# Kernel optimization log

Hardware: AMD Instinct MI355X
Metric: run time of the kernel (lower is better)

Reference implementation:

```python
import jax, jax.numpy as jnp
import numpy as np

B = 128
IN = 256
NLVL = 6
KLVL = 3
CH = 4
C = 4 * CH * CH          # 64 channels per node
OU = 8                   # out_filter_siz_u
OV = 8                   # out_filter_siz_v
NK = 2 ** KLVL           # 8 leaf nodes per axis
W_SCALE = 1.0 / 16.0     # ~1/sqrt(2*2*C) so 7 stacked relu-convs stay numerically sane


def setup_inputs() -> dict:
    key = jax.random.key(0)
    ks = jax.random.split(key, 2 * NLVL + 4)
    fx = IN // 2 ** NLVL  # 4: input patch filter size
    inp = {}
    inp["in_data"] = jax.random.normal(ks[0], (B, IN, IN, 1), jnp.float32)
    inp["in_filter"] = jax.random.normal(ks[1], (fx, fx, 1, C), jnp.float32) * W_SCALE
    inp["in_bias"] = jnp.zeros((C,), jnp.float32)
    i = 2
    for lvl in range(1, NLVL + 1):
        n = 2 ** min(lvl, KLVL)  # node grid: grows to 2^klvl then stays
        inp[f"f{lvl}"] = jax.random.normal(ks[i], (n, n, 2, 2, C, C), jnp.float32) * W_SCALE
        inp[f"b{lvl}"] = jnp.zeros((n, n, C), jnp.float32)
        i += 1
    inp["Wd"] = jax.random.normal(ks[i], (NK, NK, 2, C, OU * OV), jnp.float32) * W_SCALE
    return inp


def _node_conv(x, w, b):
    # x: [Nu,Nv,B,H,W,C]; w: [Nu,Nv,2,2,C,C]; 2x2 stride-2 VALID conv per node
    Nu, Nv, Bn, H, W, Cc = x.shape
    xr = x.reshape(Nu, Nv, Bn, H // 2, 2, W // 2, 2, Cc)
    y = jnp.einsum('uvbhxwyc,uvxyco->uvbhwo', xr, w)
    return jax.nn.relu(y + b[:, :, None, None, None, :])


def _forward(in_data, in_filter, in_bias, fs, bs, Wd):
    Bn = in_data.shape[0]
    fx, fy = in_filter.shape[0], in_filter.shape[1]
    # input interp conv: stride == kernel -> non-overlapping patch GEMM
    xr = in_data[..., 0].reshape(Bn, in_data.shape[1] // fx, fx, in_data.shape[2] // fy, fy)
    x = jax.nn.relu(jnp.einsum('bxpyq,pqc->bxyc', xr, in_filter[:, :, 0, :]) + in_bias)
    x = x[None, None]  # [1,1,B,2^nlvl,2^nlvl,C] node grid
    for lvl in range(1, NLVL + 1):
        if lvl <= KLVL:
            # children (itu,itv) read parent (itu//2, itv//2)
            x = jnp.repeat(jnp.repeat(x, 2, axis=0), 2, axis=1)
        x = _node_conv(x, fs[lvl - 1], bs[lvl - 1])
    feats = x[:, :, :, 0, 0, :]  # [NK,NK,B,C]; spatial is 1x1 at level nlvl
    out = jnp.einsum('uvbc,uvrck->uvbrk', feats, Wd)  # r in {real, imag}
    out = out.reshape(NK, NK, Bn, 2, OU, OV)
    out = jnp.transpose(out, (2, 0, 4, 1, 5, 3))  # [B,itu,ou,itv,ov,2]
    return out.reshape(Bn, NK * OU, NK * OV, 2)


def reference(in_data, in_filter, in_bias, f1, b1, f2, b2, f3, b3, f4, b4, f5, b5, f6, b6, Wd):
    fs = (f1, f2, f3, f4, f5, f6)
    bs = (b1, b2, b3, b4, b5, b6)
    return _forward(in_data, in_filter, in_bias, fs, bs, Wd)
```

## Files before the change

### kernel.cpp

```cpp
#include <hip/hip_runtime.h>
#include <hip/hip_bf16.h>
#include <cstdint>
#include <cstddef>


typedef __attribute__((ext_vector_type(8))) short short8;
typedef __attribute__((ext_vector_type(4))) float f32x4;
typedef unsigned short ushort_t;

static __device__ __forceinline__ float b2f(const __hip_bfloat16 x) {
    return __bfloat162float(x);
}
static __device__ __forceinline__ ushort_t f2bf(float x) {
    __hip_bfloat16 h = __float2bfloat16(x);
    ushort_t u;
    __builtin_memcpy(&u, &h, 2);
    return u;
}
static __device__ __forceinline__ void gl_lds16(const void* g, void* l) {
    __builtin_amdgcn_global_load_lds(
        (const __attribute__((address_space(1))) void*)g,
        (__attribute__((address_space(3))) void*)l, 16, 0, 0);
}

__global__ void k_detect(const uint32_t* __restrict__ in, int* __restrict__ flag) {
    const int t = threadIdx.x;
    const float v = __uint_as_float(in[t]);
    const bool plaus = (v == 0.0f) || (fabsf(v) > 1e-8f && fabsf(v) < 1e4f);
    const unsigned long long m = __ballot(plaus);
    if (t == 0) *flag = (__popcll(m) >= 48) ? 0 : 1;
}

__global__ __launch_bounds__(256) void k_prepw(
    const void* f1, const void* f2, const void* f3,
    const void* f4, const void* f5, const void* f6, const void* wdsrc,
    ushort_t* __restrict__ wbuf, ushort_t* __restrict__ wdbuf,
    const int* __restrict__ flag)
{
    const int isbf = *flag;
    const int gid = blockIdx.x * 256 + threadIdx.x;
    if (gid >= 630784) return;
    if (gid >= 565248) {
        const int local = gid - 565248;
        const int lane = local & 63;
        const int slot = (local >> 6) & 15;
        const int site = local >> 10;
        const int ks2 = slot >> 3, nh = slot & 7, q = lane >> 4;
        const int n = nh * 16 + (lane & 15);
        const int r = n >> 6, kk = n & 63;
        const int cbase = ks2 * 32 + q * 8;
        ushort_t pk[8];
        if (isbf) {
            const ushort_t* s = (const ushort_t*)wdsrc;
            #pragma unroll
            for (int j = 0; j < 8; j++)
                pk[j] = s[(((size_t)(site * 2 + r) * 64 + cbase + j) * 64) + kk];
        } else {
            const float* s = (const float*)wdsrc;
            #pragma unroll
            for (int j = 0; j < 8; j++)
                pk[j] = f2bf(s[(((size_t)(site * 2 + r) * 64 + cbase + j) * 64) + kk]);
        }
        *(uint4*)&wdbuf[(size_t)local * 8] = *(uint4*)pk;
        return;
    }
    const void* fsrc; int base;
    if      (gid <   8192) { fsrc = f1; base = 0;      }
    else if (gid <  40960) { fsrc = f2; base = 8192;   }
    else if (gid < 172032) { fsrc = f3; base = 40960;  }
    else if (gid < 303104) { fsrc = f4; base = 172032; }
    else if (gid < 434176) { fsrc = f5; base = 303104; }
    else                   { fsrc = f6; base = 434176; }
    const int local = gid - base;
    const int lane = local & 63;
    const int slot = (local >> 6) & 7;
    const int sitetap = local >> 9;
    const int ks = slot >> 2, nh = slot & 3, q = lane >> 4;
    const int n = (lane & 15) + nh * 16;
    const int kbase = ks * 32 + q * 8;
    ushort_t pk[8];
    if (isbf) {
        const ushort_t* s = (const ushort_t*)fsrc + (size_t)sitetap * 4096;
        #pragma unroll
        for (int j = 0; j < 8; j++) pk[j] = s[(kbase + j) * 64 + n];
    } else {
        const float* s = (const float*)fsrc + (size_t)sitetap * 4096;
        #pragma unroll
        for (int j = 0; j < 8; j++) pk[j] = f2bf(s[(kbase + j) * 64 + n]);
    }
    *(uint4*)&wbuf[(size_t)gid * 8] = *(uint4*)pk;
}

__global__ __launch_bounds__(256) void k_prepb(
    const void* b1, const void* b2, const void* b3,
    const void* b4, const void* b5, const void* b6,
    float* __restrict__ bbuf, const int* __restrict__ flag)
{
    const int isbf = *flag;
    const int gid = blockIdx.x * 256 + threadIdx.x;
    const void* src; int base;
    if      (gid <   256) { src = b1; base = 0;     }
    else if (gid <  1280) { src = b2; base = 256;   }
    else if (gid <  5376) { src = b3; base = 1280;  }
    else if (gid <  9472) { src = b4; base = 5376;  }
    else if (gid < 13568) { src = b5; base = 9472;  }
    else if (gid < 17664) { src = b6; base = 13568; }
    else return;
    const int local = gid - base;
    bbuf[gid] = isbf ? b2f(((const __hip_bfloat16*)src)[local])
                     : ((const float*)src)[local];
}

__global__ __launch_bounds__(256) void k_stage0(
    const void* __restrict__ in_data, const void* __restrict__ filt,
    const void* __restrict__ bias, __hip_bfloat16* __restrict__ x0,
    const int* __restrict__ flag, int b_off)
{
    const int isbf = *flag;
    const int blk = blockIdx.x;
    const int X  = blk & 63;
    const int bl = blk >> 6;
    const int bg = bl + b_off;

    __shared__ float sIn[4][256];
    __shared__ float sF[16][64];
    __shared__ float sB[64];

    const int t = threadIdx.x;
    const size_t srow = ((size_t)bg * 256 + (size_t)X * 4) * 256;

    if (isbf) {
        const __hip_bfloat16* src = (const __hip_bfloat16*)in_data + srow;
        #pragma unroll
        for (int i = 0; i < 4; i++) {
            int flat = i * 256 + t;
            int p = flat >> 8, col = flat & 255;
            sIn[p][col] = b2f(src[(size_t)p * 256 + col]);
        }
        const __hip_bfloat16* fsrc = (const __hip_bfloat16*)filt;
        #pragma unroll
        for (int i = 0; i < 4; i++) {
            int flat = i * 256 + t;
            sF[flat >> 6][flat & 63] = b2f(fsrc[flat]);
        }
        if (t < 64) sB[t] = b2f(((const __hip_bfloat16*)bias)[t]);
    } else {
        const float* src = (const float*)in_data + srow;
        const int p = t >> 6, c4 = (t & 63) * 4;
        *(float4*)&sIn[p][c4] = *(const float4*)(src + (size_t)p * 256 + c4);
        const float* fsrc = (const float*)filt;
        #pragma unroll
        for (int i = 0; i < 4; i++) {
            int flat = i * 256 + t;
            sF[flat >> 6][flat & 63] = fsrc[flat];
        }
        if (t < 64) sB[t] = ((const float*)bias)[t];
    }
    __syncthreads();

    const int ty = t >> 4;
    const int tc = t & 15;

    float acc[4][4];
    {
        const float4 bv = *(const float4*)&sB[tc * 4];
        #pragma unroll
        for (int yi = 0; yi < 4; yi++) {
            acc[yi][0] = bv.x; acc[yi][1] = bv.y;
            acc[yi][2] = bv.z; acc[yi][3] = bv.w;
        }
    }

    #pragma unroll
    for (int p = 0; p < 4; p++) {
        float4 rin[4], rf[4];
        #pragma unroll
        for (int yi = 0; yi < 4; yi++)
            rin[yi] = *(const float4*)&sIn[p][ty * 16 + yi * 4];
        #pragma unroll
        for (int q = 0; q < 4; q++)
            rf[q] = *(const float4*)&sF[p * 4 + q][tc * 4];
        #pragma unroll
        for (int yi = 0; yi < 4; yi++) {
            #pragma unroll
            for (int q = 0; q < 4; q++) {
                const float a = ((const float*)&rin[yi])[q];
                acc[yi][0] = fmaf(a, rf[q].x, acc[yi][0]);
                acc[yi][1] = fmaf(a, rf[q].y, acc[yi][1]);
                acc[yi][2] = fmaf(a, rf[q].z, acc[yi][2]);
                acc[yi][3] = fmaf(a, rf[q].w, acc[yi][3]);
            }
        }
    }

    ushort_t* dst = (ushort_t*)(x0 + ((size_t)bl * 64 + X) * 64 * 64);
    #pragma unroll
    for (int yi = 0; yi < 4; yi++) {
        uint2 pk;
        pk.x = (uint32_t)f2bf(fmaxf(acc[yi][0], 0.f))
             | ((uint32_t)f2bf(fmaxf(acc[yi][1], 0.f)) << 16);
        pk.y = (uint32_t)f2bf(fmaxf(acc[yi][2], 0.f))
             | ((uint32_t)f2bf(fmaxf(acc[yi][3], 0.f)) << 16);
        *(uint2*)(dst + (size_t)(ty * 4 + yi) * 64 + tc * 4) = pk;
    }
}

__global__ __launch_bounds__(256) void k_level4(
    const __hip_bfloat16* __restrict__ xin,
    const ushort_t* __restrict__ wbuf,
    const float* __restrict__ bbuf,
    __hip_bfloat16* __restrict__ xout,
    int Nv_out, int HW, int Bc, int mtiles)
{
    __shared__ ushort_t smem[20480];
    __shared__ float sBias[4][64];
    ushort_t* sA = smem;
    ushort_t* sB = smem + 4096;

    int idx = blockIdx.x;
    const int mt = idx % mtiles; idx /= mtiles;
    const int w  = idx % HW; idx /= HW;
    const int h  = idx % HW; idx /= HW;
    const int Nv_in = Nv_out >> 1;
    const int vp = idx % Nv_in;
    const int up = idx / Nv_in;

    const int t = threadIdx.x;
    const int wave = t >> 6, lane = t & 63;
    const int lm = lane & 15, lq = lane >> 4;

    {
        const int ct = t >> 6, o = t & 63;
        const int so_t = (2 * up + (ct >> 1)) * Nv_out + (2 * vp + (ct & 1));
        sBias[ct][o] = bbuf[so_t * 64 + o];
    }

    const int so = (2 * up + (wave >> 1)) * Nv_out + (2 * vp + (wave & 1));
    const int H_in = HW * 2;
    const size_t bstride = (size_t)H_in * H_in * 64;
    const size_t siteb = (size_t)(up * Nv_in + vp) * Bc * bstride;
    const ushort_t* wsite = wbuf + (size_t)so * 4 * 4096;

    const f32x4 zero = {0.f, 0.f, 0.f, 0.f};
    f32x4 acc[4][4];
    #pragma unroll
    for (int i = 0; i < 4; i++)
        #pragma unroll
        for (int j = 0; j < 4; j++) acc[i][j] = zero;

    for (int tap = 0; tap < 4; tap++) {
        const int hi = 2 * h + (tap >> 1), wi = 2 * w + (tap & 1);
        const size_t tapoff = siteb + ((size_t)hi * H_in + wi) * 64;
        #pragma unroll
        for (int s2 = 0; s2 < 2; s2++) {
            const int s = wave * 2 + s2;
            const int ks = s >> 2, mh = s & 3;
            int b = mt * 64 + lm + mh * 16;
            if (b >= Bc) b = Bc - 1;
            gl_lds16(xin + tapoff + (size_t)b * bstride + ks * 32 + lq * 8,
                     &sA[s * 512]);
        }
        const ushort_t* wt = wsite + (size_t)tap * 4096;
        #pragma unroll
        for (int s = 0; s < 8; s++) {
            gl_lds16(wt + s * 512 + lane * 8, &sB[wave * 4096 + s * 512]);
        }
        __syncthreads();

        #pragma unroll
        for (int ks = 0; ks < 2; ks++) {
            short8 bf0 = *(const short8*)&sB[wave * 4096 + (ks * 4 + 0) * 512 + lane * 8];
            short8 bf1 = *(const short8*)&sB[wave * 4096 + (ks * 4 + 1) * 512 + lane * 8];
            short8 bf2 = *(const short8*)&sB[wave * 4096 + (ks * 4 + 2) * 512 + lane * 8];
            short8 bf3 = *(const short8*)&sB[wave * 4096 + (ks * 4 + 3) * 512 + lane * 8];
            #pragma unroll
            for (int fm = 0; fm < 4; fm++) {
                short8 a = *(const short8*)&sA[(ks * 4 + fm) * 512 + lane * 8];
                acc[fm][0] = __builtin_amdgcn_mfma_f32_16x16x32_bf16(a, bf0, acc[fm][0], 0, 0, 0);
                acc[fm][1] = __builtin_amdgcn_mfma_f32_16x16x32_bf16(a, bf1, acc[fm][1], 0, 0, 0);
                acc[fm][2] = __builtin_amdgcn_mfma_f32_16x16x32_bf16(a, bf2, acc[fm][2], 0, 0, 0);
                acc[fm][3] = __builtin_amdgcn_mfma_f32_16x16x32_bf16(a, bf3, acc[fm][3], 0, 0, 0);
            }
        }
        __syncthreads();
    }

    float bv[4];
    #pragma unroll
    for (int fn = 0; fn < 4; fn++) bv[fn] = sBias[wave][fn * 16 + lm];
    ushort_t* so_buf = smem + wave * 4352;
    #pragma unroll
    for (int fm = 0; fm < 4; fm++) {
        #pragma unroll
        for (int fn = 0; fn < 4; fn++) {
            #pragma unroll
            for (int r = 0; r < 4; r++) {
                const int row = fm * 16 + lq * 4 + r;
                so_buf[row * 68 + fn * 16 + lm] =
                    f2bf(fmaxf(acc[fm][fn][r] + bv[fn], 0.f));
            }
        }
    }
    __syncthreads();

    const size_t ostride = (size_t)HW * HW * 64;
    const size_t obase = (size_t)so * Bc * ostride + ((size_t)h * HW + w) * 64;
    #pragma unroll
    for (int i = 0; i < 8; i++) {
        const int task = i * 64 + lane;
        const int oct = task & 7, row = task >> 3;
        const int b = mt * 64 + row;
        if (b < Bc) {
            *(uint4*)(xout + obase + (size_t)b * ostride + oct * 8) =
                *(const uint4*)&so_buf[row * 68 + oct * 8];
        }
    }
}

__global__ __launch_bounds__(256) void k_level1(
    const __hip_bfloat16* __restrict__ xin,
    const ushort_t* __restrict__ wbuf,
    const float* __restrict__ bbuf,
    __hip_bfloat16* __restrict__ xout,
    int Nv, int HW, int Bc, int mtiles)
{
    __shared__ ushort_t smem[12288];
    __shared__ float sBias[64];
    ushort_t* sA = smem;
    ushort_t* sB = smem + 8192;

    int idx = blockIdx.x;
    const int mt = idx % mtiles; idx /= mtiles;
    const int w  = idx % HW; idx /= HW;
    const int h  = idx % HW; idx /= HW;
    const int site = idx;

    const int t = threadIdx.x;
    const int wave = t >> 6, lane = t & 63;
    const int lm = lane & 15, lq = lane >> 4;

    if (t < 64) sBias[t] = bbuf[site * 64 + t];

    const int H_in = HW * 2;
    const size_t bstride = (size_t)H_in * H_in * 64;
    const size_t siteb = (size_t)site * Bc * bstride;
    const ushort_t* wsite = wbuf + (size_t)site * 4 * 4096;

    const f32x4 zero = {0.f, 0.f, 0.f, 0.f};
    f32x4 acc[2][4];
    #pragma unroll
    for (int i = 0; i < 2; i++)
        #pragma unroll
        for (int j = 0; j < 4; j++) acc[i][j] = zero;

    for (int tap = 0; tap < 4; tap++) {
        const int hi = 2 * h + (tap >> 1), wi = 2 * w + (tap & 1);
        const size_t tapoff = siteb + ((size_t)hi * H_in + wi) * 64;
        #pragma unroll
        for (int s2 = 0; s2 < 4; s2++) {
            const int s = wave * 4 + s2;
            const int ks = s >> 3, mh = s & 7;
            int b = mt * 128 + lm + mh * 16;
            if (b >= Bc) b = Bc - 1;
            gl_lds16(xin + tapoff + (size_t)b * bstride + ks * 32 + lq * 8,
                     &sA[s * 512]);
        }
        const ushort_t* wt = wsite + (size_t)tap * 4096;
        #pragma unroll
        for (int s2 = 0; s2 < 2; s2++) {
            const int s = wave * 2 + s2;
            gl_lds16(wt + s * 512 + lane * 8, &sB[s * 512]);
        }
        __syncthreads();

        #pragma unroll
        for (int ks = 0; ks < 2; ks++) {
            short8 bf0 = *(const short8*)&sB[(ks * 4 + 0) * 512 + lane * 8];
            short8 bf1 = *(const short8*)&sB[(ks * 4 + 1) * 512 + lane * 8];
            short8 bf2 = *(const short8*)&sB[(ks * 4 + 2) * 512 + lane * 8];
            short8 bf3 = *(const short8*)&sB[(ks * 4 + 3) * 512 + lane * 8];
            #pragma unroll
            for (int fml = 0; fml < 2; fml++) {
                short8 a = *(const short8*)&sA[(ks * 8 + wave * 2 + fml) * 512 + lane * 8];
                acc[fml][0] = __builtin_amdgcn_mfma_f32_16x16x32_bf16(a, bf0, acc[fml][0], 0, 0, 0);
                acc[fml][1] = __builtin_amdgcn_mfma_f32_16x16x32_bf16(a, bf1, acc[fml][1], 0, 0, 0);
                acc[fml][2] = __builtin_amdgcn_mfma_f32_16x16x32_bf16(a, bf2, acc[fml][2], 0, 0, 0);
                acc[fml][3] = __builtin_amdgcn_mfma_f32_16x16x32_bf16(a, bf3, acc[fml][3], 0, 0, 0);
            }
        }
        __syncthreads();
    }

    float bv[4];
    #pragma unroll
    for (int fn = 0; fn < 4; fn++) bv[fn] = sBias[fn * 16 + lm];
    ushort_t* so_buf = smem;
    #pragma unroll
    for (int fml = 0; fml < 2; fml++) {
        #pragma unroll
        for (int fn = 0; fn < 4; fn++) {
            #pragma unroll
            for (int r = 0; r < 4; r++) {
                const int row = wave * 32 + fml * 16 + lq * 4 + r;
                so_buf[row * 68 + fn * 16 + lm] =
                    f2bf(fmaxf(acc[fml][fn][r] + bv[fn], 0.f));
            }
        }
    }
    __syncthreads();

    const size_t ostride = (size_t)HW * HW * 64;
    const size_t obase = (size_t)site * Bc * ostride + ((size_t)h * HW + w) * 64;
    #pragma unroll
    for (int i = 0; i < 4; i++) {
        const int task = i * 256 + t;
        const int oct = task & 7, row = task >> 3;
        const int b = mt * 128 + row;
        if (b < Bc) {
            *(uint4*)(xout + obase + (size_t)b * ostride + oct * 8) =
                *(const uint4*)&so_buf[row * 68 + oct * 8];
        }
    }
}

__global__ __launch_bounds__(256) void k_tail(
    const __hip_bfloat16* __restrict__ xin,
    const ushort_t* __restrict__ w6,
    const float* __restrict__ b6,
    const ushort_t* __restrict__ wd,
    void* __restrict__ out,
    const int* __restrict__ flag, int Bc, int b_off)
{
    const int isbf = *flag;
    const int site = blockIdx.x;
    const int u = site >> 3, v = site & 7;

    __shared__ ushort_t sA[16 * 512];
    __shared__ ushort_t sB1[8 * 512];
    __shared__ ushort_t sMid[128 * 72];
    __shared__ float sBias[64];

    const int t = threadIdx.x;
    const int wave = t >> 6, lane = t & 63;
    const int lm = lane & 15, lq = lane >> 4;

    if (t < 64) sBias[t] = b6[site * 64 + t];

    const f32x4 zero = {0.f, 0.f, 0.f, 0.f};
    f32x4 acc1[2][4];
    #pragma unroll
    for (int i = 0; i < 2; i++)
        #pragma unroll
        for (int j = 0; j < 4; j++) acc1[i][j] = zero;

    const size_t abase = (size_t)site * Bc * 256;

    for (int chunk = 0; chunk < 4; chunk++) {
        #pragma unroll
        for (int s2 = 0; s2 < 4; s2++) {
            const int s = wave * 4 + s2;
            const int ks = s >> 3, mh = s & 7;
            int b = mh * 16 + lm;
            if (b >= Bc) b = Bc - 1;
            gl_lds16(xin + abase + (size_t)b * 256 + chunk * 64 + ks * 32 + lq * 8,
                     &sA[s * 512]);
        }
        const ushort_t* wt = w6 + (size_t)(site * 4 + chunk) * 4096;
        #pragma unroll
        for (int s2 = 0; s2 < 2; s2++) {
            const int s = wave * 2 + s2;
            gl_lds16(wt + s * 512 + lane * 8, &sB1[s * 512]);
        }
        __syncthreads();

        #pragma unroll
        for (int ks = 0; ks < 2; ks++) {
            short8 bf0 = *(const short8*)&sB1[(ks * 4 + 0) * 512 + lane * 8];
            short8 bf1 = *(const short8*)&sB1[(ks * 4 + 1) * 512 + lane * 8];
            short8 bf2 = *(const short8*)&sB1[(ks * 4 + 2) * 512 + lane * 8];
            short8 bf3 = *(const short8*)&sB1[(ks * 4 + 3) * 512 + lane * 8];
            #pragma unroll
            for (int fml = 0; fml < 2; fml++) {
                short8 a = *(const short8*)&sA[(ks * 8 + wave * 2 + fml) * 512 + lane * 8];
                acc1[fml][0] = __builtin_amdgcn_mfma_f32_16x16x32_bf16(a, bf0, acc1[fml][0], 0, 0, 0);
                acc1[fml][1] = __builtin_amdgcn_mfma_f32_16x16x32_bf16(a, bf1, acc1[fml][1], 0, 0, 0);
                acc1[fml][2] = __builtin_amdgcn_mfma_f32_16x16x32_bf16(a, bf2, acc1[fml][2], 0, 0, 0);
                acc1[fml][3] = __builtin_amdgcn_mfma_f32_16x16x32_bf16(a, bf3, acc1[fml][3], 0, 0, 0);
            }
        }
        __syncthreads();
    }

    float bv[4];
    #pragma unroll
    for (int fn = 0; fn < 4; fn++) bv[fn] = sBias[fn * 16 + lm];
    #pragma unroll
    for (int fml = 0; fml < 2; fml++) {
        #pragma unroll
        for (int fn = 0; fn < 4; fn++) {
            #pragma unroll
            for (int r = 0; r < 4; r++) {
                const int row = wave * 32 + fml * 16 + lq * 4 + r;
                sMid[row * 72 + fn * 16 + lm] =
                    f2bf(fmaxf(acc1[fml][fn][r] + bv[fn], 0.f));
            }
        }
    }
    #pragma unroll
    for (int s2 = 0; s2 < 4; s2++) {
        const int s = wave * 4 + s2;
        gl_lds16(wd + ((size_t)(site * 16 + s) * 64 + lane) * 8, &sA[s * 512]);
    }
    __syncthreads();

    f32x4 acc2[2][8];
    #pragma unroll
    for (int i = 0; i < 2; i++)
        #pragma unroll
        for (int j = 0; j < 8; j++) acc2[i][j] = zero;

    #pragma unroll
    for (int ks2 = 0; ks2 < 2; ks2++) {
        short8 a20 = *(const short8*)&sMid[((wave * 2 + 0) * 16 + lm) * 72 + ks2 * 32 + lq * 8];
        short8 a21 = *(const short8*)&sMid[((wave * 2 + 1) * 16 + lm) * 72 + ks2 * 32 + lq * 8];
        #pragma unroll
        for (int nh = 0; nh < 8; nh++) {
            short8 bv2 = *(const short8*)&sA[(ks2 * 8 + nh) * 512 + lane * 8];
            acc2[0][nh] = __builtin_amdgcn_mfma_f32_16x16x32_bf16(a20, bv2, acc2[0][nh], 0, 0, 0);
            acc2[1][nh] = __builtin_amdgcn_mfma_f32_16x16x32_bf16(a21, bv2, acc2[1][nh], 0, 0, 0);
        }
    }

    #pragma unroll
    for (int fml = 0; fml < 2; fml++) {
        #pragma unroll
        for (int nh = 0; nh < 8; nh++) {
            const int n = nh * 16 + lm;
            const int r = n >> 6, ou = (n >> 3) & 7, ov = n & 7;
            const size_t obase =
                (((size_t)0 * 64 + (u * 8 + ou)) * 64 + (v * 8 + ov)) * 2 + r;
            #pragma unroll
            for (int reg = 0; reg < 4; reg++) {
                const int brow = wave * 32 + fml * 16 + lq * 4 + reg;
                if (brow < Bc) {
                    const size_t oidx = obase + (size_t)(b_off + brow) * 8192;
                    if (isbf) ((__hip_bfloat16*)out)[oidx] =
                        __float2bfloat16(acc2[fml][nh][reg]);
                    else ((float*)out)[oidx] = acc2[fml][nh][reg];
                }
            }
        }
    }
}

extern "C" void kernel_launch(void* const* d_in, const int* in_sizes, int n_in,
                              void* d_out, int out_size, void* d_ws, size_t ws_size,
                              hipStream_t stream)
{
    (void)in_sizes; (void)n_in; (void)out_size;

    const void* in_data = d_in[0];
    const void* filt    = d_in[1];
    const void* bias0   = d_in[2];
    const void* fl[7];
    const void* bl[7];
    for (int l = 1; l <= 6; l++) {
        fl[l] = d_in[1 + 2 * l];
        bl[l] = d_in[2 + 2 * l];
    }
    const void* Wd = d_in[15];

    const int Bfull = 128;
    const size_t perB = (size_t)64 * 64 * 64;

    const size_t wbufBytes  = 565248ull * 16;
    const size_t wdbufBytes = 65536ull * 16;
    const size_t bbufBytes  = 17664ull * 4;
    const size_t headBytes  = 256 + wbufBytes + wdbufBytes + bbufBytes;

    const size_t avail = ws_size > headBytes ? ws_size - headBytes : 0;
    int Bc = 0;
    for (int c = 128; c >= 1; c >>= 1) {
        if ((size_t)2 * c * perB * sizeof(__hip_bfloat16) <= avail) { Bc = c; break; }
    }
    if (Bc == 0) return;

    int* flag = (int*)d_ws;
    ushort_t* wbuf  = (ushort_t*)((char*)d_ws + 256);
    ushort_t* wdbuf = (ushort_t*)((char*)d_ws + 256 + wbufBytes);
    float* bbuf = (float*)((char*)d_ws + 256 + wbufBytes + wdbufBytes);
    __hip_bfloat16* bufA = (__hip_bfloat16*)((char*)d_ws + headBytes);
    __hip_bfloat16* bufB = bufA + (size_t)Bc * perB;

    static const size_t w_off[7] = {0, 0, 65536, 327680, 1376256, 2424832, 3473408};
    static const int    b_off_tab[7] = {0, 0, 256, 1280, 5376, 9472, 13568};

    k_detect<<<dim3(1), 64, 0, stream>>>((const uint32_t*)in_data, flag);
    k_prepw<<<dim3(2464), 256, 0, stream>>>(fl[1], fl[2], fl[3], fl[4], fl[5], fl[6],
                                            Wd, wbuf, wdbuf, flag);
    k_prepb<<<dim3(69), 256, 0, stream>>>(bl[1], bl[2], bl[3], bl[4], bl[5], bl[6], bbuf, flag);

    const int mt4 = (Bc + 63) / 64;
    const int mt1 = (Bc + 127) / 128;

    for (int b_off = 0; b_off < Bfull; b_off += Bc) {
        k_stage0<<<dim3(Bc * 64), 256, 0, stream>>>(in_data, filt, bias0, bufA, flag, b_off);

        __hip_bfloat16* cur = bufA;
        __hip_bfloat16* nxt = bufB;
        for (int lvl = 1; lvl <= 5; lvl++) {
            const int Nu = 1 << (lvl < 3 ? lvl : 3);
            const int H  = 64 >> lvl;
            if (lvl <= 3) {
                const int Nv_in = Nu >> 1;
                dim3 grid(Nv_in * Nv_in * H * H * mt4);
                k_level4<<<grid, 256, 0, stream>>>(cur, wbuf + w_off[lvl],
                    bbuf + b_off_tab[lvl], nxt, Nu, H, Bc, mt4);
            } else {
                dim3 grid(Nu * Nu * H * H * mt1);
                k_level1<<<grid, 256, 0, stream>>>(cur, wbuf + w_off[lvl],
                    bbuf + b_off_tab[lvl], nxt, Nu, H, Bc, mt1);
            }
            __hip_bfloat16* tmp = cur; cur = nxt; nxt = tmp;
        }

        k_tail<<<dim3(64), 256, 0, stream>>>(cur, wbuf + w_off[6],
            bbuf + b_off_tab[6], wdbuf, d_out, flag, Bc, b_off);
    }
}
```

Before: 266.6 us.

## Fuse levels 4-6 and the output GEMM into one per-site kernel; merge prep kernels

Replaces the separate level-4 and level-5 conv kernels and the tail kernel with one kernel, k_f456. Each block owns one leaf site and a 32-batch tile and keeps the level-4, level-5 and level-6 intermediates in LDS, so those activations no longer round-trip through global memory between launches. The detect, weight-prep and bias-prep kernels are also merged into a single launch. In exchange, the fused kernel uses about 150 KB of LDS with one block per CU, and its grid is only 64 × ceil(Bc/32) blocks, which may leave CUs idle and give weaker latency hiding.

New measurement: 248.8 us. 1.07x faster.

```diff
diff --git a/kernel.cpp b/kernel.cpp
--- a/kernel.cpp
+++ b/kernel.cpp
@@ -22,24 +22,46 @@
         (const __attribute__((address_space(1))) void*)g,
         (__attribute__((address_space(3))) void*)l, 16, 0, 0);
 }
-
-__global__ void k_detect(const uint32_t* __restrict__ in, int* __restrict__ flag) {
-    const int t = threadIdx.x;
-    const float v = __uint_as_float(in[t]);
-    const bool plaus = (v == 0.0f) || (fabsf(v) > 1e-8f && fabsf(v) < 1e4f);
-    const unsigned long long m = __ballot(plaus);
-    if (t == 0) *flag = (__popcll(m) >= 48) ? 0 : 1;
-}
-
-__global__ __launch_bounds__(256) void k_prepw(
+#define WAIT_LGKM0() __builtin_amdgcn_s_waitcnt(0xC07F)
+#define WAIT_VM0()   __builtin_amdgcn_s_waitcnt(0x0F70)
+
+__global__ __launch_bounds__(256) void k_prep(
+    const uint32_t* __restrict__ in_words,
     const void* f1, const void* f2, const void* f3,
     const void* f4, const void* f5, const void* f6, const void* wdsrc,
+    const void* b1, const void* b2, const void* b3,
+    const void* b4, const void* b5, const void* b6,
     ushort_t* __restrict__ wbuf, ushort_t* __restrict__ wdbuf,
-    const int* __restrict__ flag)
+    float* __restrict__ bbuf, int* __restrict__ flag)
 {
-    const int isbf = *flag;
-    const int gid = blockIdx.x * 256 + threadIdx.x;
-    if (gid >= 630784) return;
+    __shared__ int sflag;
+    const int t = threadIdx.x;
+    if (t < 64) {
+        const float v = __uint_as_float(in_words[t]);
+        const bool plaus = (v == 0.0f) || (fabsf(v) > 1e-8f && fabsf(v) < 1e4f);
+        const unsigned long long m = __ballot(plaus);
+        if (t == 0) sflag = (__popcll(m) >= 48) ? 0 : 1;
+    }
+    __syncthreads();
+    const int isbf = sflag;
+    const int gid = blockIdx.x * 256 + t;
+    if (blockIdx.x == 0 && t == 0) *flag = isbf;
+
+    if (gid >= 648448) return;
+    if (gid >= 630784) {
+        const int bg = gid - 630784;
+        const void* src; int base;
+        if      (bg <   256) { src = b1; base = 0;     }
+        else if (bg <  1280) { src = b2; base = 256;   }
+        else if (bg <  5376) { src = b3; base = 1280;  }
+        else if (bg <  9472) { src = b4; base = 5376;  }
+        else if (bg < 13568) { src = b5; base = 9472;  }
+        else                 { src = b6; base = 13568; }
+        const int local = bg - base;
+        bbuf[bg] = isbf ? b2f(((const __hip_bfloat16*)src)[local])
+                        : ((const float*)src)[local];
+        return;
+    }
     if (gid >= 565248) {
         const int local = gid - 565248;
         const int lane = local & 63;
@@ -91,26 +113,6 @@
     *(uint4*)&wbuf[(size_t)gid * 8] = *(uint4*)pk;
 }
 
-__global__ __launch_bounds__(256) void k_prepb(
-    const void* b1, const void* b2, const void* b3,
-    const void* b4, const void* b5, const void* b6,
-    float* __restrict__ bbuf, const int* __restrict__ flag)
-{
-    const int isbf = *flag;
-    const int gid = blockIdx.x * 256 + threadIdx.x;
-    const void* src; int base;
-    if      (gid <   256) { src = b1; base = 0;     }
-    else if (gid <  1280) { src = b2; base = 256;   }
-    else if (gid <  5376) { src = b3; base = 1280;  }
-    else if (gid <  9472) { src = b4; base = 5376;  }
-    else if (gid < 13568) { src = b5; base = 9472;  }
-    else if (gid < 17664) { src = b6; base = 13568; }
-    else return;
-    const int local = gid - base;
-    bbuf[gid] = isbf ? b2f(((const __hip_bfloat16*)src)[local])
-                     : ((const float*)src)[local];
-}
-
 __global__ __launch_bounds__(256) void k_stage0(
     const void* __restrict__ in_data, const void* __restrict__ filt,
     const void* __restrict__ bias, __hip_bfloat16* __restrict__ x0,
@@ -317,236 +319,215 @@
     }
 }
 
-__global__ __launch_bounds__(256) void k_level1(
+__global__ __launch_bounds__(256, 1) void k_f456(
     const __hip_bfloat16* __restrict__ xin,
-    const ushort_t* __restrict__ wbuf,
-    const float* __restrict__ bbuf,
-    __hip_bfloat16* __restrict__ xout,
-    int Nv, int HW, int Bc, int mtiles)
-{
-    __shared__ ushort_t smem[12288];
-    __shared__ float sBias[64];
-    ushort_t* sA = smem;
-    ushort_t* sB = smem + 8192;
-
-    int idx = blockIdx.x;
-    const int mt = idx % mtiles; idx /= mtiles;
-    const int w  = idx % HW; idx /= HW;
-    const int h  = idx % HW; idx /= HW;
-    const int site = idx;
-
-    const int t = threadIdx.x;
-    const int wave = t >> 6, lane = t & 63;
-    const int lm = lane & 15, lq = lane >> 4;
-
-    if (t < 64) sBias[t] = bbuf[site * 64 + t];
-
-    const int H_in = HW * 2;
-    const size_t bstride = (size_t)H_in * H_in * 64;
-    const size_t siteb = (size_t)site * Bc * bstride;
-    const ushort_t* wsite = wbuf + (size_t)site * 4 * 4096;
-
-    const f32x4 zero = {0.f, 0.f, 0.f, 0.f};
-    f32x4 acc[2][4];
-    #pragma unroll
-    for (int i = 0; i < 2; i++)
-        #pragma unroll
-        for (int j = 0; j < 4; j++) acc[i][j] = zero;
-
-    for (int tap = 0; tap < 4; tap++) {
-        const int hi = 2 * h + (tap >> 1), wi = 2 * w + (tap & 1);
-        const size_t tapoff = siteb + ((size_t)hi * H_in + wi) * 64;
-        #pragma unroll
-        for (int s2 = 0; s2 < 4; s2++) {
-            const int s = wave * 4 + s2;
-            const int ks = s >> 3, mh = s & 7;
-            int b = mt * 128 + lm + mh * 16;
-            if (b >= Bc) b = Bc - 1;
-            gl_lds16(xin + tapoff + (size_t)b * bstride + ks * 32 + lq * 8,
-                     &sA[s * 512]);
-        }
-        const ushort_t* wt = wsite + (size_t)tap * 4096;
-        #pragma unroll
-        for (int s2 = 0; s2 < 2; s2++) {
-            const int s = wave * 2 + s2;
-            gl_lds16(wt + s * 512 + lane * 8, &sB[s * 512]);
-        }
-        __syncthreads();
-
-        #pragma unroll
-        for (int ks = 0; ks < 2; ks++) {
-            short8 bf0 = *(const short8*)&sB[(ks * 4 + 0) * 512 + lane * 8];
-            short8 bf1 = *(const short8*)&sB[(ks * 4 + 1) * 512 + lane * 8];
-            short8 bf2 = *(const short8*)&sB[(ks * 4 + 2) * 512 + lane * 8];
-            short8 bf3 = *(const short8*)&sB[(ks * 4 + 3) * 512 + lane * 8];
-            #pragma unroll
-            for (int fml = 0; fml < 2; fml++) {
-                short8 a = *(const short8*)&sA[(ks * 8 + wave * 2 + fml) * 512 + lane * 8];
-                acc[fml][0] = __builtin_amdgcn_mfma_f32_16x16x32_bf16(a, bf0, acc[fml][0], 0, 0, 0);
-                acc[fml][1] = __builtin_amdgcn_mfma_f32_16x16x32_bf16(a, bf1, acc[fml][1], 0, 0, 0);
-                acc[fml][2] = __builtin_amdgcn_mfma_f32_16x16x32_bf16(a, bf2, acc[fml][2], 0, 0, 0);
-                acc[fml][3] = __builtin_amdgcn_mfma_f32_16x16x32_bf16(a, bf3, acc[fml][3], 0, 0, 0);
-            }
-        }
-        __syncthreads();
-    }
-
-    float bv[4];
-    #pragma unroll
-    for (int fn = 0; fn < 4; fn++) bv[fn] = sBias[fn * 16 + lm];
-    ushort_t* so_buf = smem;
-    #pragma unroll
-    for (int fml = 0; fml < 2; fml++) {
-        #pragma unroll
-        for (int fn = 0; fn < 4; fn++) {
-            #pragma unroll
-            for (int r = 0; r < 4; r++) {
-                const int row = wave * 32 + fml * 16 + lq * 4 + r;
-                so_buf[row * 68 + fn * 16 + lm] =
-                    f2bf(fmaxf(acc[fml][fn][r] + bv[fn], 0.f));
-            }
-        }
-    }
-    __syncthreads();
-
-    const size_t ostride = (size_t)HW * HW * 64;
-    const size_t obase = (size_t)site * Bc * ostride + ((size_t)h * HW + w) * 64;
-    #pragma unroll
-    for (int i = 0; i < 4; i++) {
-        const int task = i * 256 + t;
-        const int oct = task & 7, row = task >> 3;
-        const int b = mt * 128 + row;
-        if (b < Bc) {
-            *(uint4*)(xout + obase + (size_t)b * ostride + oct * 8) =
-                *(const uint4*)&so_buf[row * 68 + oct * 8];
-        }
-    }
-}
-
-__global__ __launch_bounds__(256) void k_tail(
-    const __hip_bfloat16* __restrict__ xin,
-    const ushort_t* __restrict__ w6,
+    const ushort_t* __restrict__ w4, const ushort_t* __restrict__ w5,
+    const ushort_t* __restrict__ w6, const ushort_t* __restrict__ wd,
+    const float* __restrict__ b4, const float* __restrict__ b5,
     const float* __restrict__ b6,
-    const ushort_t* __restrict__ wd,
-    void* __restrict__ out,
-    const int* __restrict__ flag, int Bc, int b_off)
+    void* __restrict__ out, const int* __restrict__ flag,
+    int Bc, int b_off, int mtiles)
 {
     const int isbf = *flag;
-    const int site = blockIdx.x;
+    const int bx = blockIdx.x;
+    const int mt = bx % mtiles;
+    const int site = bx / mtiles;
     const int u = site >> 3, v = site & 7;
 
-    __shared__ ushort_t sA[16 * 512];
-    __shared__ ushort_t sB1[8 * 512];
-    __shared__ ushort_t sMid[128 * 72];
-    __shared__ float sBias[64];
+    __shared__ ushort_t smem[74752];
+    __shared__ float sBias[192];
 
     const int t = threadIdx.x;
-    const int wave = t >> 6, lane = t & 63;
+    const int wv = t >> 6, lane = t & 63;
     const int lm = lane & 15, lq = lane >> 4;
 
-    if (t < 64) sBias[t] = b6[site * 64 + t];
+    if (t < 64) {
+        sBias[t]       = b4[site * 64 + t];
+        sBias[64 + t]  = b5[site * 64 + t];
+        sBias[128 + t] = b6[site * 64 + t];
+    }
+
+    {
+        const ushort_t* w4s = w4 + (size_t)site * 16384;
+        const ushort_t* w5s = w5 + (size_t)site * 16384;
+        #pragma unroll
+        for (int s2 = 0; s2 < 8; s2++) {
+            const int s = wv * 8 + s2;
+            gl_lds16(w4s + s * 512 + lane * 8, &smem[s * 512]);
+            gl_lds16(w5s + s * 512 + lane * 8, &smem[16384 + s * 512]);
+        }
+    }
+    __syncthreads();
 
     const f32x4 zero = {0.f, 0.f, 0.f, 0.f};
-    f32x4 acc1[2][4];
-    #pragma unroll
-    for (int i = 0; i < 2; i++)
-        #pragma unroll
-        for (int j = 0; j < 4; j++) acc1[i][j] = zero;
-
-    const size_t abase = (size_t)site * Bc * 256;
-
-    for (int chunk = 0; chunk < 4; chunk++) {
+    const int h5 = wv >> 1, w5p = wv & 1;
+    ushort_t* mid1w = smem + 32768 + wv * 8448;
+    ushort_t* Aw = smem + 66560 + wv * 2048;
+    const size_t sb = (size_t)site * Bc;
+
+    for (int i = 0; i < 4; i++) {
+        const int h4 = 2 * h5 + (i >> 1), w4p = 2 * w5p + (i & 1);
+        f32x4 acc[2][4];
+        #pragma unroll
+        for (int a_ = 0; a_ < 2; a_++)
+            #pragma unroll
+            for (int b_ = 0; b_ < 4; b_++) acc[a_][b_] = zero;
+
+        for (int tap = 0; tap < 4; tap++) {
+            const int h3 = 2 * h4 + (tap >> 1), w3 = 2 * w4p + (tap & 1);
+            WAIT_LGKM0();
+            #pragma unroll
+            for (int sl = 0; sl < 4; sl++) {
+                const int ks = sl >> 1, mh = sl & 1;
+                int b = mt * 32 + mh * 16 + lm;
+                if (b >= Bc) b = Bc - 1;
+                gl_lds16(xin + (sb + b) * 4096 + (h3 * 8 + w3) * 64 + ks * 32 + lq * 8,
+                         &Aw[sl * 512]);
+            }
+            WAIT_VM0();
+            #pragma unroll
+            for (int ks = 0; ks < 2; ks++) {
+                #pragma unroll
+                for (int fm = 0; fm < 2; fm++) {
+                    short8 a = *(const short8*)&Aw[(ks * 2 + fm) * 512 + lane * 8];
+                    #pragma unroll
+                    for (int fn = 0; fn < 4; fn++) {
+                        short8 bfr = *(const short8*)&smem[(tap * 8 + ks * 4 + fn) * 512 + lane * 8];
+                        acc[fm][fn] = __builtin_amdgcn_mfma_f32_16x16x32_bf16(a, bfr, acc[fm][fn], 0, 0, 0);
+                    }
+                }
+            }
+        }
+        #pragma unroll
+        for (int fm = 0; fm < 2; fm++) {
+            #pragma unroll
+            for (int fn = 0; fn < 4; fn++) {
+                #pragma unroll
+                for (int r = 0; r < 4; r++) {
+                    const int m = fm * 16 + lq * 4 + r;
+                    const int ch = fn * 16 + lm;
+                    mid1w[m * 264 + i * 64 + ch] =
+                        f2bf(fmaxf(acc[fm][fn][r] + sBias[ch], 0.f));
+                }
+            }
+        }
+    }
+
+    {
+        f32x4 acc2[2][4];
+        #pragma unroll
+        for (int a_ = 0; a_ < 2; a_++)
+            #pragma unroll
+            for (int b_ = 0; b_ < 4; b_++) acc2[a_][b_] = zero;
+
+        #pragma unroll
+        for (int i = 0; i < 4; i++) {
+            #pragma unroll
+            for (int ks = 0; ks < 2; ks++) {
+                short8 a0 = *(const short8*)&mid1w[lm * 264 + i * 64 + ks * 32 + lq * 8];
+                short8 a1 = *(const short8*)&mid1w[(16 + lm) * 264 + i * 64 + ks * 32 + lq * 8];
+                #pragma unroll
+                for (int fn = 0; fn < 4; fn++) {
+                    short8 bfr = *(const short8*)&smem[16384 + (i * 8 + ks * 4 + fn) * 512 + lane * 8];
+                    acc2[0][fn] = __builtin_amdgcn_mfma_f32_16x16x32_bf16(a0, bfr, acc2[0][fn], 0, 0, 0);
+                    acc2[1][fn] = __builtin_amdgcn_mfma_f32_16x16x32_bf16(a1, bfr, acc2[1][fn], 0, 0, 0);
+                }
+            }
+        }
+        #pragma unroll
+        for (int fm = 0; fm < 2; fm++) {
+            #pragma unroll
+            for (int fn = 0; fn < 4; fn++) {
+                #pragma unroll
+                for (int r = 0; r < 4; r++) {
+                    const int m = fm * 16 + lq * 4 + r;
+                    const int ch = fn * 16 + lm;
+                    mid1w[m * 72 + ch] =
+                        f2bf(fmaxf(acc2[fm][fn][r] + sBias[64 + ch], 0.f));
+                }
+            }
+        }
+    }
+    __syncthreads();
+
+    {
+        const ushort_t* w6s = w6 + (size_t)site * 16384;
+        const ushort_t* wds = wd + (size_t)site * 8192;
+        #pragma unroll
+        for (int s2 = 0; s2 < 8; s2++) {
+            const int s = wv * 8 + s2;
+            gl_lds16(w6s + s * 512 + lane * 8, &smem[s * 512]);
+        }
         #pragma unroll
         for (int s2 = 0; s2 < 4; s2++) {
-            const int s = wave * 4 + s2;
-            const int ks = s >> 3, mh = s & 7;
-            int b = mh * 16 + lm;
-            if (b >= Bc) b = Bc - 1;
-            gl_lds16(xin + abase + (size_t)b * 256 + chunk * 64 + ks * 32 + lq * 8,
-                     &sA[s * 512]);
-        }
-        const ushort_t* wt = w6 + (size_t)(site * 4 + chunk) * 4096;
-        #pragma unroll
-        for (int s2 = 0; s2 < 2; s2++) {
-            const int s = wave * 2 + s2;
-            gl_lds16(wt + s * 512 + lane * 8, &sB1[s * 512]);
-        }
-        __syncthreads();
-
+            const int s = wv * 4 + s2;
+            gl_lds16(wds + s * 512 + lane * 8, &smem[16384 + s * 512]);
+        }
+    }
+    __syncthreads();
+
+    {
+        f32x4 acc3[2];
+        acc3[0] = zero; acc3[1] = zero;
+        #pragma unroll
+        for (int tap = 0; tap < 4; tap++) {
+            const ushort_t* sl = smem + 32768 + tap * 8448;
+            #pragma unroll
+            for (int ks = 0; ks < 2; ks++) {
+                short8 a0 = *(const short8*)&sl[lm * 72 + ks * 32 + lq * 8];
+                short8 a1 = *(const short8*)&sl[(16 + lm) * 72 + ks * 32 + lq * 8];
+                short8 bfr = *(const short8*)&smem[(tap * 8 + ks * 4 + wv) * 512 + lane * 8];
+                acc3[0] = __builtin_amdgcn_mfma_f32_16x16x32_bf16(a0, bfr, acc3[0], 0, 0, 0);
+                acc3[1] = __builtin_amdgcn_mfma_f32_16x16x32_bf16(a1, bfr, acc3[1], 0, 0, 0);
+            }
+        }
+        ushort_t* mid3 = smem + 66560;
+        #pragma unroll
+        for (int fm = 0; fm < 2; fm++) {
+            #pragma unroll
+            for (int r = 0; r < 4; r++) {
+                const int m = fm * 16 + lq * 4 + r;
+                const int ch = wv * 16 + lm;
+                mid3[m * 72 + ch] =
+                    f2bf(fmaxf(acc3[fm][r] + sBias[128 + ch], 0.f));
+            }
+        }
+    }
+    __syncthreads();
+
+    {
+        const ushort_t* mid3 = smem + 66560;
+        f32x4 acc4[2][2];
+        acc4[0][0] = zero; acc4[0][1] = zero; acc4[1][0] = zero; acc4[1][1] = zero;
         #pragma unroll
         for (int ks = 0; ks < 2; ks++) {
-            short8 bf0 = *(const short8*)&sB1[(ks * 4 + 0) * 512 + lane * 8];
-            short8 bf1 = *(const short8*)&sB1[(ks * 4 + 1) * 512 + lane * 8];
-            short8 bf2 = *(const short8*)&sB1[(ks * 4 + 2) * 512 + lane * 8];
-            short8 bf3 = *(const short8*)&sB1[(ks * 4 + 3) * 512 + lane * 8];
-            #pragma unroll
-            for (int fml = 0; fml < 2; fml++) {
-                short8 a = *(const short8*)&sA[(ks * 8 + wave * 2 + fml) * 512 + lane * 8];
-                acc1[fml][0] = __builtin_amdgcn_mfma_f32_16x16x32_bf16(a, bf0, acc1[fml][0], 0, 0, 0);
-                acc1[fml][1] = __builtin_amdgcn_mfma_f32_16x16x32_bf16(a, bf1, acc1[fml][1], 0, 0, 0);
-                acc1[fml][2] = __builtin_amdgcn_mfma_f32_16x16x32_bf16(a, bf2, acc1[fml][2], 0, 0, 0);
-                acc1[fml][3] = __builtin_amdgcn_mfma_f32_16x16x32_bf16(a, bf3, acc1[fml][3], 0, 0, 0);
-            }
-        }
-        __syncthreads();
-    }
-
-    float bv[4];
-    #pragma unroll
-    for (int fn = 0; fn < 4; fn++) bv[fn] = sBias[fn * 16 + lm];
-    #pragma unroll
-    for (int fml = 0; fml < 2; fml++) {
-        #pragma unroll
-        for (int fn = 0; fn < 4; fn++) {
-            #pragma unroll
-            for (int r = 0; r < 4; r++) {
-                const int row = wave * 32 + fml * 16 + lq * 4 + r;
-                sMid[row * 72 + fn * 16 + lm] =
-                    f2bf(fmaxf(acc1[fml][fn][r] + bv[fn], 0.f));
-            }
-        }
-    }
-    #pragma unroll
-    for (int s2 = 0; s2 < 4; s2++) {
-        const int s = wave * 4 + s2;
-        gl_lds16(wd + ((size_t)(site * 16 + s) * 64 + lane) * 8, &sA[s * 512]);
-    }
-    __syncthreads();
-
-    f32x4 acc2[2][8];
-    #pragma unroll
-    for (int i = 0; i < 2; i++)
-        #pragma unroll
-        for (int j = 0; j < 8; j++) acc2[i][j] = zero;
-
-    #pragma unroll
-    for (int ks2 = 0; ks2 < 2; ks2++) {
-        short8 a20 = *(const short8*)&sMid[((wave * 2 + 0) * 16 + lm) * 72 + ks2 * 32 + lq * 8];
-        short8 a21 = *(const short8*)&sMid[((wave * 2 + 1) * 16 + lm) * 72 + ks2 * 32 + lq * 8];
-        #pragma unroll
-        for (int nh = 0; nh < 8; nh++) {
-            short8 bv2 = *(const short8*)&sA[(ks2 * 8 + nh) * 512 + lane * 8];
-            acc2[0][nh] = __builtin_amdgcn_mfma_f32_16x16x32_bf16(a20, bv2, acc2[0][nh], 0, 0, 0);
-            acc2[1][nh] = __builtin_amdgcn_mfma_f32_16x16x32_bf16(a21, bv2, acc2[1][nh], 0, 0, 0);
-        }
-    }
-
-    #pragma unroll
-    for (int fml = 0; fml < 2; fml++) {
-        #pragma unroll
-        for (int nh = 0; nh < 8; nh++) {
-            const int n = nh * 16 + lm;
-            const int r = n >> 6, ou = (n >> 3) & 7, ov = n & 7;
-            const size_t obase =
-                (((size_t)0 * 64 + (u * 8 + ou)) * 64 + (v * 8 + ov)) * 2 + r;
-            #pragma unroll
-            for (int reg = 0; reg < 4; reg++) {
-                const int brow = wave * 32 + fml * 16 + lq * 4 + reg;
-                if (brow < Bc) {
-                    const size_t oidx = obase + (size_t)(b_off + brow) * 8192;
-                    if (isbf) ((__hip_bfloat16*)out)[oidx] =
-                        __float2bfloat16(acc2[fml][nh][reg]);
-                    else ((float*)out)[oidx] = acc2[fml][nh][reg];
+            short8 a0 = *(const short8*)&mid3[lm * 72 + ks * 32 + lq * 8];
+            short8 a1 = *(const short8*)&mid3[(16 + lm) * 72 + ks * 32 + lq * 8];
+            #pragma unroll
+            for (int n2 = 0; n2 < 2; n2++) {
+                const int nh = 2 * wv + n2;
+                short8 bfr = *(const short8*)&smem[16384 + (ks * 8 + nh) * 512 + lane * 8];
+                acc4[0][n2] = __builtin_amdgcn_mfma_f32_16x16x32_bf16(a0, bfr, acc4[0][n2], 0, 0, 0);
+                acc4[1][n2] = __builtin_amdgcn_mfma_f32_16x16x32_bf16(a1, bfr, acc4[1][n2], 0, 0, 0);
+            }
+        }
+        #pragma unroll
+        for (int fm = 0; fm < 2; fm++) {
+            #pragma unroll
+            for (int n2 = 0; n2 < 2; n2++) {
+                const int n = (2 * wv + n2) * 16 + lm;
+                const int rr = n >> 6, ou = (n >> 3) & 7, ov = n & 7;
+                const size_t obase =
+                    (((size_t)(u * 8 + ou)) * 64 + (v * 8 + ov)) * 2 + rr;
+                #pragma unroll
+                for (int reg = 0; reg < 4; reg++) {
+                    const int brow = mt * 32 + fm * 16 + lq * 4 + reg;
+                    if (brow < Bc) {
+                        const size_t oidx = obase + (size_t)(b_off + brow) * 8192;
+                        if (isbf) ((__hip_bfloat16*)out)[oidx] =
+                            __float2bfloat16(acc4[fm][n2][reg]);
+                        else ((float*)out)[oidx] = acc4[fm][n2][reg];
+                    }
                 }
             }
         }
@@ -595,36 +576,33 @@
     static const size_t w_off[7] = {0, 0, 65536, 327680, 1376256, 2424832, 3473408};
     static const int    b_off_tab[7] = {0, 0, 256, 1280, 5376, 9472, 13568};
 
-    k_detect<<<dim3(1), 64, 0, stream>>>((const uint32_t*)in_data, flag);
-    k_prepw<<<dim3(2464), 256, 0, stream>>>(fl[1], fl[2], fl[3], fl[4], fl[5], fl[6],
-                                            Wd, wbuf, wdbuf, flag);
-    k_prepb<<<dim3(69), 256, 0, stream>>>(bl[1], bl[2], bl[3], bl[4], bl[5], bl[6], bbuf, flag);
+    k_prep<<<dim3(2533), 256, 0, stream>>>(
+        (const uint32_t*)in_data,
+        fl[1], fl[2], fl[3], fl[4], fl[5], fl[6], Wd,
+        bl[1], bl[2], bl[3], bl[4], bl[5], bl[6],
+        wbuf, wdbuf, bbuf, flag);
 
     const int mt4 = (Bc + 63) / 64;
-    const int mt1 = (Bc + 127) / 128;
+    const int mt32 = (Bc + 31) / 32;
 
     for (int b_off = 0; b_off < Bfull; b_off += Bc) {
         k_stage0<<<dim3(Bc * 64), 256, 0, stream>>>(in_data, filt, bias0, bufA, flag, b_off);
 
         __hip_bfloat16* cur = bufA;
         __hip_bfloat16* nxt = bufB;
-        for (int lvl = 1; lvl <= 5; lvl++) {
-            const int Nu = 1 << (lvl < 3 ? lvl : 3);
+        for (int lvl = 1; lvl <= 3; lvl++) {
+            const int Nu = 1 << lvl;
             const int H  = 64 >> lvl;
-            if (lvl <= 3) {
-                const int Nv_in = Nu >> 1;
-                dim3 grid(Nv_in * Nv_in * H * H * mt4);
-                k_level4<<<grid, 256, 0, stream>>>(cur, wbuf + w_off[lvl],
-                    bbuf + b_off_tab[lvl], nxt, Nu, H, Bc, mt4);
-            } else {
-                dim3 grid(Nu * Nu * H * H * mt1);
-                k_level1<<<grid, 256, 0, stream>>>(cur, wbuf + w_off[lvl],
-                    bbuf + b_off_tab[lvl], nxt, Nu, H, Bc, mt1);
-            }
+            const int Nv_in = Nu >> 1;
+            dim3 grid(Nv_in * Nv_in * H * H * mt4);
+            k_level4<<<grid, 256, 0, stream>>>(cur, wbuf + w_off[lvl],
+                bbuf + b_off_tab[lvl], nxt, Nu, H, Bc, mt4);
             __hip_bfloat16* tmp = cur; cur = nxt; nxt = tmp;
         }
 
-        k_tail<<<dim3(64), 256, 0, stream>>>(cur, wbuf + w_off[6],
-            bbuf + b_off_tab[6], wdbuf, d_out, flag, Bc, b_off);
-    }
-}
+        k_f456<<<dim3(64 * mt32), 256, 0, stream>>>(cur,
+            wbuf + w_off[4], wbuf + w_off[5], wbuf + w_off[6], wdbuf,
+            bbuf + b_off_tab[4], bbuf + b_off_tab[5], bbuf + b_off_tab[6],
+            d_out, flag, Bc, b_off, mt32);
+    }
+}
```
